# Kernel optimization log

Hardware: AMD Instinct MI355X
Metric: run time of the kernel (lower is better)

## Reference

```python
import jax, jax.numpy as jnp
import numpy as np
from jax import lax

ROUTE_SCALE = 1.0
TOPK = 2


def conv2d(x, w, stride=1, pad=1):
    # x: [B, Cin, H, W], w: [Cout, Cin, kh, kw]
    return lax.conv_general_dilated(
        x, w, window_strides=(stride, stride),
        padding=[(pad, pad), (pad, pad)],
        dimension_numbers=("NCHW", "OIHW", "NCHW"))


def setup_inputs() -> dict:
    key = jax.random.key(0)
    ks = jax.random.split(key, 6)
    B, Cin, Cout, H, W, E = 8, 32, 32, 256, 256, 8
    x = jax.random.normal(ks[0], (B, Cin, H, W), dtype=jnp.float32)
    gate_w = jax.random.normal(ks[1], (E, Cin, 3, 3), dtype=jnp.float32) * 0.05
    gate_bias = jnp.zeros((E,), dtype=jnp.float32)  # load-balance bias buffer (zero in eval)
    expert_w = jax.random.normal(ks[2], (E, Cout, Cin, 3, 3), dtype=jnp.float32) * 0.05
    expert_b = jax.random.normal(ks[3], (E, Cout), dtype=jnp.float32) * 0.05
    shared_w = jax.random.normal(ks[4], (Cout, Cin, 3, 3), dtype=jnp.float32) * 0.05
    shared_b = jax.random.normal(ks[5], (Cout,), dtype=jnp.float32) * 0.05
    return {"x": x, "gate_w": gate_w, "gate_bias": gate_bias,
            "expert_w": expert_w, "expert_b": expert_b,
            "shared_w": shared_w, "shared_b": shared_b}


def reference(x, gate_w, gate_bias, expert_w, expert_b, shared_w, shared_b):
    B, Cin, H, W = x.shape
    E, Cout = expert_w.shape[0], expert_w.shape[1]
    # ---- Gate: sigmoid(conv) -> per-pixel top-k over expert channel dim ----
    scores = jax.nn.sigmoid(conv2d(x, gate_w))                 # [B, E, H, W]
    biased = scores + gate_bias[None, :, None, None]
    st = jnp.moveaxis(scores, 1, -1)                            # [B, H, W, E]
    bt = jnp.moveaxis(biased, 1, -1)
    _, idx = lax.top_k(bt, TOPK)                                # [B, H, W, K]
    w = jnp.take_along_axis(st, idx, axis=-1)                   # gather raw scores
    w = jax.nn.softmax(w, axis=-1) * ROUTE_SCALE                # [B, H, W, K]
    # dense per-expert routing weight: sum_k w_k * onehot(idx_k)
    onehot = jax.nn.one_hot(idx, E, dtype=x.dtype)              # [B, H, W, K, E]
    dense = jnp.einsum('bhwk,bhwke->bhwe', w, onehot)           # [B, H, W, E]
    dense = jnp.moveaxis(dense, -1, 1)                          # [B, E, H, W]
    # ---- All expert convs as one stacked conv, masked accumulate ----
    ew = expert_w.reshape(E * Cout, Cin, 3, 3)
    eo = conv2d(x, ew) + expert_b.reshape(-1)[None, :, None, None]
    eo = eo.reshape(B, E, Cout, H, W)
    out = jnp.einsum('bechw,behw->bchw', eo, dense)
    # ---- Shared expert ----
    out = out + conv2d(x, shared_w) + shared_b[None, :, None, None]
    return out
```

## Files before the change

### kernel.cpp

```cpp
#include <hip/hip_runtime.h>

typedef __attribute__((ext_vector_type(8)))  short bf16x8;
typedef __attribute__((ext_vector_type(16))) float f32x16;

#define XIM (32*256*256)

__device__ __forceinline__ short f2bf(float f){
    unsigned int u = __builtin_bit_cast(unsigned int, f);
    u += 0x7fffu + ((u >> 16) & 1u);
    return (short)(u >> 16);
}
__device__ __forceinline__ float bf2f(short s){
    unsigned int u = ((unsigned int)(unsigned short)s) << 16;
    return __builtin_bit_cast(float, u);
}
__device__ __forceinline__ void glds16(const short* g, short* l){
    __builtin_amdgcn_global_load_lds(
        (const __attribute__((address_space(1))) unsigned int*)g,
        (__attribute__((address_space(3))) unsigned int*)l,
        16, 0, 0);
}

__global__ __launch_bounds__(256) void prep_weights(const float* __restrict__ ew,
                                                    const float* __restrict__ sw,
                                                    const float* __restrict__ ebv,
                                                    const float* __restrict__ sbv,
                                                    short* __restrict__ wt2){
    int i = blockIdx.x * 256 + threadIdx.x;
    if(i < 73728){
        int c7  = i & 7;
        int col = (i >> 3) & 31;
        int cio = (i >> 8) & 3;
        int rest = i >> 10;
        int tap = rest % 9;
        int es  = rest / 9;
        int ci  = cio*8 + c7;
        float v = ew[((es*32 + col)*32 + ci)*9 + tap] + sw[(col*32 + ci)*9 + tap];
        wt2[i] = f2bf(v);
    } else {
        int j = i - 73728, c = j >> 4, k = j & 15;
        float v = (k < 8) ? (ebv[k*32 + c] + sbv[c]) : 0.f;
        wt2[i] = f2bf(v);
    }
}

__global__ __launch_bounds__(256) void gate_kernel(const float* __restrict__ x,
                                                   const float* __restrict__ gw,
                                                   const float* __restrict__ gb,
                                                   short* __restrict__ route){
    __shared__ float xs[32][272];
    int raw = blockIdx.x;
    int wg  = (raw & 7)*128 + (raw >> 3);
    int b   = wg >> 7;
    int y0  = (wg & 127) * 2;
    int t   = threadIdx.x;
    int wv  = t >> 6, lane = t & 63;
    const float* xim = x + (size_t)b * XIM;

    if(t < 64){
        int s2 = t >> 1;
        if(t & 1) xs[s2][260] = 0.f; else xs[s2][3] = 0.f;
    }

    float g[2][8];
    #pragma unroll
    for(int pr=0;pr<2;++pr)
        #pragma unroll
        for(int e=0;e<8;++e) g[pr][e] = 0.f;

    for(int cc=0; cc<4; ++cc){
        __syncthreads();
        #pragma unroll
        for(int sg=0; sg<8; ++sg){
            int seg = wv*8 + sg;
            int r4  = seg >> 3;
            int ci  = (seg & 7) + cc*8;
            int yy  = y0 - 1 + r4;
            const float* xr = xim + ((size_t)ci*256 + yy)*256;
            float4 v = make_float4(0.f,0.f,0.f,0.f);
            if(yy >= 0 && yy < 256) v = *(const float4*)(xr + lane*4);
            *(float4*)(&xs[seg][4 + lane*4]) = v;
        }
        __syncthreads();
        #pragma unroll
        for(int ci=0; ci<8; ++ci){
            float sv[4][3];
            #pragma unroll
            for(int r4=0;r4<4;++r4){
                sv[r4][0] = xs[r4*8+ci][t+3];
                sv[r4][1] = xs[r4*8+ci][t+4];
                sv[r4][2] = xs[r4*8+ci][t+5];
            }
            const float* gwp = gw + (cc*8 + ci)*9;
            #pragma unroll
            for(int e=0;e<8;++e){
                #pragma unroll
                for(int kh=0;kh<3;++kh){
                    #pragma unroll
                    for(int kw=0;kw<3;++kw){
                        float wval = gwp[e*288 + kh*3 + kw];
                        g[0][e] = fmaf(sv[kh][kw],   wval, g[0][e]);
                        g[1][e] = fmaf(sv[kh+1][kw], wval, g[1][e]);
                    }
                }
            }
        }
    }

    #pragma unroll
    for(int pr=0; pr<2; ++pr){
        float v1b=-1e30f, v2b=-1e30f, v3b=-1e30f, r1=0.f, r2=0.f; int i1=-1, i2=-1;
        #pragma unroll
        for(int e=0;e<8;e++){
            float se = 1.f/(1.f + expf(-g[pr][e]));
            float be = se + gb[e];
            if(be > v1b){ v3b=v2b; v2b=v1b; r2=r1; i2=i1; v1b=be; r1=se; i1=e; }
            else if(be > v2b){ v3b=v2b; v2b=be; r2=se; i2=e; }
            else if(be > v3b){ v3b=be; }
        }
        if(v2b - v3b < 2e-5f){
            int y = y0 + pr;
            double gd[8];
            #pragma unroll
            for(int e=0;e<8;e++) gd[e] = 0.0;
            for(int ci=0; ci<32; ++ci){
                for(int kh=0; kh<3; ++kh){
                    int yy = y + kh - 1;
                    if(yy < 0 || yy >= 256) continue;
                    const float* xr = xim + ((size_t)ci*256 + yy)*256;
                    for(int kw=0; kw<3; ++kw){
                        int xx = t + kw - 1;
                        if(xx < 0 || xx >= 256) continue;
                        double xv = (double)xr[xx];
                        const float* gwp = gw + ci*9 + kh*3 + kw;
                        #pragma unroll
                        for(int e=0;e<8;e++) gd[e] += xv * (double)gwp[e*288];
                    }
                }
            }
            double b1=-1e30, b2=-1e30; double rr1=0.0, rr2=0.0; int j1=-1, j2=-1;
            #pragma unroll
            for(int e=0;e<8;e++){
                double sd = 1.0/(1.0 + exp(-gd[e]));
                double bd = sd + (double)gb[e];
                if(bd > b1){ b2=b1; rr2=rr1; j2=j1; b1=bd; rr1=sd; j1=e; }
                else if(bd > b2){ b2=bd; rr2=sd; j2=e; }
            }
            i1=j1; i2=j2; r1=(float)rr1; r2=(float)rr2;
        }
        float m  = fmaxf(r1, r2);
        float e1 = expf(r1-m), e2 = expf(r2-m);
        float inv = 1.f/(e1+e2);
        float w1 = e1*inv, w2 = e2*inv;
        bf16x8 ov;
        #pragma unroll
        for(int e=0;e<8;e++){
            float dv = (e==i1) ? w1 : ((e==i2) ? w2 : 0.f);
            ov[e] = f2bf(dv);
        }
        *(bf16x8*)(route + ((size_t)(b*256 + y0 + pr)*256 + t)*8) = ov;
    }
}

__global__ __launch_bounds__(512, 2) void moe_main(const float* __restrict__ x,
                                                   const short* __restrict__ wt2,
                                                   const short* __restrict__ route,
                                                   float* __restrict__ out){
    __shared__ __align__(16) short wlds[73728];
    __shared__ __align__(16) short xt[10*2*34*8];
    int raw = blockIdx.x;
    int wg  = (raw & 7)*256 + (raw >> 3);
    int b   = wg >> 8;
    int y0  = ((wg >> 3) & 31) * 8;
    int x0  = (wg & 7) * 32;
    int t   = threadIdx.x;
    int wv  = t >> 6, l = t & 63, col = l & 31, hi = l >> 5;

    #pragma unroll
    for(int j=0;j<18;++j){
        int c = wv + 8*j;
        glds16(wt2 + c*512 + l*8, wlds + c*512);
    }

    const float* xim = x + (size_t)b*XIM;
    int yy = y0 + wv;
    bf16x8 biasA = *(const bf16x8*)(wt2 + 73728 + col*16 + hi*8);
    bf16x8 rfrag = *(const bf16x8*)(route + ((size_t)(b*256 + yy)*256 + x0 + col)*8);

    bf16x8 Bf[3][2][3];
    #pragma unroll
    for(int hf=0; hf<2; ++hf){
        if(hf) __syncthreads();
        {
            int px = t & 31, grp = t >> 5;
            #pragma unroll
            for(int i=0;i<10;++i){
                int pair = i*16 + grp;
                int row = pair >> 4, cil = pair & 15, ci = hf*16 + cil;
                int ry = y0 - 1 + row, xx = x0 - 1 + px;
                float v = (ry>=0 && ry<256 && xx>=0 && xx<256) ? xim[((size_t)ci*256+ry)*256+xx] : 0.f;
                xt[((row*2 + (cil>>3))*34 + px)*8 + (cil&7)] = f2bf(v);
            }
            if(t < 320){
                int pair = t >> 1, px2 = 32 + (t & 1);
                int row = pair >> 4, cil = pair & 15, ci = hf*16 + cil;
                int ry = y0 - 1 + row, xx = x0 - 1 + px2;
                float v = (ry>=0 && ry<256 && xx>=0 && xx<256) ? xim[((size_t)ci*256+ry)*256+xx] : 0.f;
                xt[((row*2 + (cil>>3))*34 + px2)*8 + (cil&7)] = f2bf(v);
            }
        }
        __syncthreads();
        #pragma unroll
        for(int kh=0;kh<3;++kh)
            #pragma unroll
            for(int kw=0;kw<3;++kw)
                Bf[kh][hf][kw] = *(const bf16x8*)(&xt[(((wv+kh)*2 + hi)*34 + col + kw)*8]);
    }

    f32x16 z = {};
    f32x16 oa = __builtin_amdgcn_mfma_f32_32x32x16_bf16(biasA, rfrag, z, 0,0,0);

    #pragma unroll
    for(int es=0; es<8; ++es){
        f32x16 acc = {};
        #pragma unroll
        for(int tap=0; tap<9; ++tap){
            const int kh = tap/3, kw = tap - kh*3;
            #pragma unroll
            for(int hf=0; hf<2; ++hf){
                bf16x8 a = *(const bf16x8*)(&wlds[(((es*9 + tap)*4 + hf*2 + hi)*32 + col)*8]);
                acc = __builtin_amdgcn_mfma_f32_32x32x16_bf16(a, Bf[kh][hf][kw], acc, 0,0,0);
            }
        }
        float d = bf2f(rfrag[es]);
        #pragma unroll
        for(int r=0;r<16;r++) oa[r] += d*acc[r];
    }

    float* ob = out + (size_t)b*XIM;
    #pragma unroll
    for(int r=0;r<16;r++){
        int c = hi*4 + (r&3) + 8*(r>>2);
        ob[((size_t)c*256 + yy)*256 + x0 + col] = oa[r];
    }
}

extern "C" void kernel_launch(void* const* d_in, const int* in_sizes, int n_in,
                              void* d_out, int out_size, void* d_ws, size_t ws_size,
                              hipStream_t stream){
    (void)in_sizes; (void)n_in; (void)out_size; (void)ws_size;
    const float* x   = (const float*)d_in[0];
    const float* gw  = (const float*)d_in[1];
    const float* gb  = (const float*)d_in[2];
    const float* ew  = (const float*)d_in[3];
    const float* ebv = (const float*)d_in[4];
    const float* sw  = (const float*)d_in[5];
    const float* sbv = (const float*)d_in[6];
    float* out = (float*)d_out;

    short* route = (short*)d_ws;
    short* wt2   = route + (size_t)8*256*256*8;

    prep_weights<<<dim3(290),  dim3(256), 0, stream>>>(ew, sw, ebv, sbv, wt2);
    gate_kernel <<<dim3(1024), dim3(256), 0, stream>>>(x, gw, gb, route);
    moe_main    <<<dim3(2048), dim3(512), 0, stream>>>(x, wt2, route, out);
}
```

Before: 237.6 us.

## Make moe_main persistent over x-tiles and double-buffer gate input staging

moe_main now launches 256 blocks, each looping over 8 column tiles of an 8-row strip. The 147KB bf16 expert-weight LDS load then happens once per block instead of once per 32x8 tile, and the x-tile staging packs 8 channels per thread into one vector store. Separately, the gate kernel double-buffers its LDS staging in 4-channel chunks so global loads overlap the FMA work. The risk is that 256 blocks may underfill the GPU (256 CUs, 2 blocks/CU allowed) and that serialized tiles lose latency hiding.

```diff
diff --git a/kernel.cpp b/kernel.cpp
--- a/kernel.cpp
+++ b/kernel.cpp
@@ -48,7 +48,7 @@
                                                    const float* __restrict__ gw,
                                                    const float* __restrict__ gb,
                                                    short* __restrict__ route){
-    __shared__ float xs[32][272];
+    __shared__ float xs[2][16][272];
     int raw = blockIdx.x;
     int wg  = (raw & 7)*128 + (raw >> 3);
     int b   = wg >> 7;
@@ -58,40 +58,45 @@
     const float* xim = x + (size_t)b * XIM;
 
     if(t < 64){
-        int s2 = t >> 1;
-        if(t & 1) xs[s2][260] = 0.f; else xs[s2][3] = 0.f;
-    }
-
-    float g[2][8];
-    #pragma unroll
-    for(int pr=0;pr<2;++pr)
-        #pragma unroll
-        for(int e=0;e<8;++e) g[pr][e] = 0.f;
-
-    for(int cc=0; cc<4; ++cc){
-        __syncthreads();
-        #pragma unroll
-        for(int sg=0; sg<8; ++sg){
-            int seg = wv*8 + sg;
-            int r4  = seg >> 3;
-            int ci  = (seg & 7) + cc*8;
+        int bufi = t >> 5, s2 = (t >> 1) & 15;
+        if(t & 1) xs[bufi][s2][260] = 0.f; else xs[bufi][s2][3] = 0.f;
+    }
+
+    auto STAGE = [&](int cc, int bufi){
+        #pragma unroll
+        for(int sg=0; sg<4; ++sg){
+            int seg = wv*4 + sg;
+            int r4  = seg >> 2, cid = seg & 3;
+            int ci  = cc*4 + cid;
             int yy  = y0 - 1 + r4;
             const float* xr = xim + ((size_t)ci*256 + yy)*256;
             float4 v = make_float4(0.f,0.f,0.f,0.f);
             if(yy >= 0 && yy < 256) v = *(const float4*)(xr + lane*4);
-            *(float4*)(&xs[seg][4 + lane*4]) = v;
-        }
-        __syncthreads();
-        #pragma unroll
-        for(int ci=0; ci<8; ++ci){
+            *(float4*)(&xs[bufi][seg][4 + lane*4]) = v;
+        }
+    };
+
+    float g[2][8];
+    #pragma unroll
+    for(int pr=0;pr<2;++pr)
+        #pragma unroll
+        for(int e=0;e<8;++e) g[pr][e] = 0.f;
+
+    STAGE(0, 0);
+    __syncthreads();
+    for(int cc=0; cc<8; ++cc){
+        if(cc < 7) STAGE(cc+1, (cc+1)&1);
+        const int bufi = cc & 1;
+        #pragma unroll
+        for(int cid=0; cid<4; ++cid){
             float sv[4][3];
             #pragma unroll
             for(int r4=0;r4<4;++r4){
-                sv[r4][0] = xs[r4*8+ci][t+3];
-                sv[r4][1] = xs[r4*8+ci][t+4];
-                sv[r4][2] = xs[r4*8+ci][t+5];
-            }
-            const float* gwp = gw + (cc*8 + ci)*9;
+                sv[r4][0] = xs[bufi][r4*4+cid][t+3];
+                sv[r4][1] = xs[bufi][r4*4+cid][t+4];
+                sv[r4][2] = xs[bufi][r4*4+cid][t+5];
+            }
+            const float* gwp = gw + (cc*4 + cid)*9;
             #pragma unroll
             for(int e=0;e<8;++e){
                 #pragma unroll
@@ -105,6 +110,7 @@
                 }
             }
         }
+        __syncthreads();
     }
 
     #pragma unroll
@@ -169,10 +175,9 @@
     __shared__ __align__(16) short wlds[73728];
     __shared__ __align__(16) short xt[10*2*34*8];
     int raw = blockIdx.x;
-    int wg  = (raw & 7)*256 + (raw >> 3);
-    int b   = wg >> 8;
-    int y0  = ((wg >> 3) & 31) * 8;
-    int x0  = (wg & 7) * 32;
+    int wg  = (raw & 7)*32 + (raw >> 3);
+    int b   = wg >> 5;
+    int y0  = (wg & 31) * 8;
     int t   = threadIdx.x;
     int wv  = t >> 6, l = t & 63, col = l & 31, hi = l >> 5;
 
@@ -183,65 +188,81 @@
     }
 
     const float* xim = x + (size_t)b*XIM;
+    float* ob = out + (size_t)b*XIM;
     int yy = y0 + wv;
     bf16x8 biasA = *(const bf16x8*)(wt2 + 73728 + col*16 + hi*8);
-    bf16x8 rfrag = *(const bf16x8*)(route + ((size_t)(b*256 + yy)*256 + x0 + col)*8);
-
-    bf16x8 Bf[3][2][3];
-    #pragma unroll
-    for(int hf=0; hf<2; ++hf){
-        if(hf) __syncthreads();
-        {
-            int px = t & 31, grp = t >> 5;
-            #pragma unroll
-            for(int i=0;i<10;++i){
-                int pair = i*16 + grp;
-                int row = pair >> 4, cil = pair & 15, ci = hf*16 + cil;
-                int ry = y0 - 1 + row, xx = x0 - 1 + px;
-                float v = (ry>=0 && ry<256 && xx>=0 && xx<256) ? xim[((size_t)ci*256+ry)*256+xx] : 0.f;
-                xt[((row*2 + (cil>>3))*34 + px)*8 + (cil&7)] = f2bf(v);
-            }
-            if(t < 320){
-                int pair = t >> 1, px2 = 32 + (t & 1);
-                int row = pair >> 4, cil = pair & 15, ci = hf*16 + cil;
-                int ry = y0 - 1 + row, xx = x0 - 1 + px2;
-                float v = (ry>=0 && ry<256 && xx>=0 && xx<256) ? xim[((size_t)ci*256+ry)*256+xx] : 0.f;
-                xt[((row*2 + (cil>>3))*34 + px2)*8 + (cil&7)] = f2bf(v);
-            }
-        }
-        __syncthreads();
-        #pragma unroll
-        for(int kh=0;kh<3;++kh)
-            #pragma unroll
-            for(int kw=0;kw<3;++kw)
-                Bf[kh][hf][kw] = *(const bf16x8*)(&xt[(((wv+kh)*2 + hi)*34 + col + kw)*8]);
-    }
-
-    f32x16 z = {};
-    f32x16 oa = __builtin_amdgcn_mfma_f32_32x32x16_bf16(biasA, rfrag, z, 0,0,0);
-
-    #pragma unroll
-    for(int es=0; es<8; ++es){
-        f32x16 acc = {};
-        #pragma unroll
-        for(int tap=0; tap<9; ++tap){
-            const int kh = tap/3, kw = tap - kh*3;
-            #pragma unroll
-            for(int hf=0; hf<2; ++hf){
-                bf16x8 a = *(const bf16x8*)(&wlds[(((es*9 + tap)*4 + hf*2 + hi)*32 + col)*8]);
-                acc = __builtin_amdgcn_mfma_f32_32x32x16_bf16(a, Bf[kh][hf][kw], acc, 0,0,0);
-            }
-        }
-        float d = bf2f(rfrag[es]);
-        #pragma unroll
-        for(int r=0;r<16;r++) oa[r] += d*acc[r];
-    }
-
-    float* ob = out + (size_t)b*XIM;
-    #pragma unroll
-    for(int r=0;r<16;r++){
-        int c = hi*4 + (r&3) + 8*(r>>2);
-        ob[((size_t)c*256 + yy)*256 + x0 + col] = oa[r];
+
+    for(int tile=0; tile<8; ++tile){
+        int x0 = tile*32;
+        bf16x8 rfrag = *(const bf16x8*)(route + ((size_t)(b*256 + yy)*256 + x0 + col)*8);
+        bf16x8 Bf[3][2][3];
+        #pragma unroll
+        for(int hf=0; hf<2; ++hf){
+            __syncthreads();
+            #pragma unroll
+            for(int i=0;i<2;++i){
+                int u = t + i*512;
+                if(u < 640){
+                    int px = u & 31, rc = u >> 5;
+                    int row = rc >> 1, cic = rc & 1;
+                    int cib = hf*16 + cic*8;
+                    int ry = y0 - 1 + row, xx = x0 - 1 + px;
+                    bool ok = (ry>=0 && ry<256 && xx>=0 && xx<256);
+                    bf16x8 pk;
+                    #pragma unroll
+                    for(int j2=0;j2<8;++j2){
+                        float v = ok ? xim[((size_t)(cib+j2)*256 + ry)*256 + xx] : 0.f;
+                        pk[j2] = f2bf(v);
+                    }
+                    *(bf16x8*)(&xt[((row*2 + cic)*34 + px)*8]) = pk;
+                }
+            }
+            if(t < 40){
+                int pxh = 32 + (t & 1), rc = t >> 1;
+                int row = rc >> 1, cic = rc & 1;
+                int cib = hf*16 + cic*8;
+                int ry = y0 - 1 + row, xx = x0 - 1 + pxh;
+                bool ok = (ry>=0 && ry<256 && xx>=0 && xx<256);
+                bf16x8 pk;
+                #pragma unroll
+                for(int j2=0;j2<8;++j2){
+                    float v = ok ? xim[((size_t)(cib+j2)*256 + ry)*256 + xx] : 0.f;
+                    pk[j2] = f2bf(v);
+                }
+                *(bf16x8*)(&xt[((row*2 + cic)*34 + pxh)*8]) = pk;
+            }
+            __syncthreads();
+            #pragma unroll
+            for(int kh=0;kh<3;++kh)
+                #pragma unroll
+                for(int kw=0;kw<3;++kw)
+                    Bf[kh][hf][kw] = *(const bf16x8*)(&xt[(((wv+kh)*2 + hi)*34 + col + kw)*8]);
+        }
+
+        f32x16 z = {};
+        f32x16 oa = __builtin_amdgcn_mfma_f32_32x32x16_bf16(biasA, rfrag, z, 0,0,0);
+        #pragma unroll
+        for(int es=0; es<8; ++es){
+            f32x16 acc = {};
+            #pragma unroll
+            for(int tap=0; tap<9; ++tap){
+                const int kh = tap/3, kw = tap - kh*3;
+                #pragma unroll
+                for(int hf=0; hf<2; ++hf){
+                    bf16x8 a = *(const bf16x8*)(&wlds[(((es*9 + tap)*4 + hf*2 + hi)*32 + col)*8]);
+                    acc = __builtin_amdgcn_mfma_f32_32x32x16_bf16(a, Bf[kh][hf][kw], acc, 0,0,0);
+                }
+            }
+            float d = bf2f(rfrag[es]);
+            #pragma unroll
+            for(int r=0;r<16;r++) oa[r] += d*acc[r];
+        }
+
+        #pragma unroll
+        for(int r=0;r<16;r++){
+            int c = hi*4 + (r&3) + 8*(r>>2);
+            ob[((size_t)c*256 + yy)*256 + x0 + col] = oa[r];
+        }
     }
 }
 
@@ -263,5 +284,5 @@
 
     prep_weights<<<dim3(290),  dim3(256), 0, stream>>>(ew, sw, ebv, sbv, wt2);
     gate_kernel <<<dim3(1024), dim3(256), 0, stream>>>(x, gw, gb, route);
-    moe_main    <<<dim3(2048), dim3(512), 0, stream>>>(x, wt2, route, out);
-}
+    moe_main    <<<dim3(256),  dim3(512), 0, stream>>>(x, wt2, route, out);
+}
```

Result: slower. 252.3 us (+6.2%).
